# Optimization experiments

Measured on AMD Instinct MI355X. Metric: run time of the kernel, lower is better.

## Reference

```python
import jax, jax.numpy as jnp
import numpy as np

B, N, D, H, DM = 4, 1024, 1024, 16, 4096
DH = D // H
SCALE = DH ** -0.5
EPS = 1e-5


def layer_norm(x, g, b):
    mu = jnp.mean(x, axis=-1, keepdims=True)
    var = jnp.mean((x - mu) ** 2, axis=-1, keepdims=True)
    return (x - mu) * jax.lax.rsqrt(var + EPS) * g + b


def mha(q_in, k_in, v_in, Wq, bq, Wk, bk, Wv, bv, Wp, bp):
    # weights stored (in, out); torch Linear equivalent y = x @ W + b
    q = (q_in @ Wq + bq).reshape(B, -1, H, DH).transpose(0, 2, 1, 3)  # (B,H,Nq,DH)
    k = (k_in @ Wk + bk).reshape(B, -1, H, DH).transpose(0, 2, 1, 3)
    v = (v_in @ Wv + bv).reshape(B, -1, H, DH).transpose(0, 2, 1, 3)
    attn = jax.nn.softmax(jnp.einsum('bhqd,bhkd->bhqk', q, k) * SCALE, axis=-1)
    x = jnp.einsum('bhqk,bhkd->bhqd', attn, v).transpose(0, 2, 1, 3).reshape(B, -1, D)
    return x @ Wp + bp


def setup_inputs() -> dict:
    key = jax.random.key(0)
    ks = jax.random.split(key, 32)
    s = 0.02
    inp = {
        'tokens_enc': jax.random.normal(ks[0], (B, N, D), jnp.float32),
        'tokens_dec': jax.random.normal(ks[1], (B, N, D), jnp.float32),
        'PE_enc': jax.random.normal(ks[2], (B, N, D), jnp.float32),
        'PE_dec': jax.random.normal(ks[3], (B, N, D), jnp.float32),
    }
    names = ['sa_Wq', 'sa_Wk', 'sa_Wv', 'sa_Wp', 'ca_Wq', 'ca_Wk', 'ca_Wv', 'ca_Wp']
    for i, n in enumerate(names):
        inp[n] = jax.random.normal(ks[4 + i], (D, D), jnp.float32) * s
        inp[n.replace('W', 'b')] = jnp.zeros((D,), jnp.float32)
    inp['mlp_W1'] = jax.random.normal(ks[12], (D, DM), jnp.float32) * s
    inp['mlp_b1'] = jnp.zeros((DM,), jnp.float32)
    inp['mlp_W2'] = jax.random.normal(ks[13], (DM, D), jnp.float32) * s
    inp['mlp_b2'] = jnp.zeros((D,), jnp.float32)
    for i in (1, 2, 3):
        inp[f'ln{i}_g'] = jnp.ones((D,), jnp.float32)
        inp[f'ln{i}_b'] = jnp.zeros((D,), jnp.float32)
    return inp


def reference(tokens_enc, tokens_dec, PE_enc, PE_dec,
              sa_Wq, sa_bq, sa_Wk, sa_bk, sa_Wv, sa_bv, sa_Wp, sa_bp,
              ca_Wq, ca_bq, ca_Wk, ca_bk, ca_Wv, ca_bv, ca_Wp, ca_bp,
              mlp_W1, mlp_b1, mlp_W2, mlp_b2,
              ln1_g, ln1_b, ln2_g, ln2_b, ln3_g, ln3_b):
    # SA (pre-norm): q=k=ln(x)+PE_dec, v=ln(x)
    x2 = layer_norm(tokens_dec, ln1_g, ln1_b)
    qk = x2 + PE_dec
    tokens_dec = tokens_dec + mha(qk, qk, x2, sa_Wq, sa_bq, sa_Wk, sa_bk, sa_Wv, sa_bv, sa_Wp, sa_bp)
    # CA: q=ln(x)+PE_dec, k=enc+PE_enc, v=enc
    x2 = layer_norm(tokens_dec, ln2_g, ln2_b)
    tokens_dec = tokens_dec + mha(x2 + PE_dec, tokens_enc + PE_enc, tokens_enc,
                                  ca_Wq, ca_bq, ca_Wk, ca_bk, ca_Wv, ca_bv, ca_Wp, ca_bp)
    # FFD
    x2 = layer_norm(tokens_dec, ln3_g, ln3_b)
    h = jax.nn.gelu(x2 @ mlp_W1 + mlp_b1, approximate=False)
    return tokens_dec + (h @ mlp_W2 + mlp_b2)
```

## Files before the change

### kernel.cpp

```cpp
#include <hip/hip_runtime.h>
#include <hip/hip_bf16.h>
#include <math.h>

#define B_ 4
#define N_ 1024
#define D_ 1024
#define H_ 16
#define DH_ 64
#define DM_ 4096
#define NT_ (B_*N_)
#define EPS_ 1e-5f
#define SCALE_ 0.125f
#define CEXP_ 0.1803368801111244f

typedef unsigned short u16;
typedef short s16x8 __attribute__((ext_vector_type(8)));
typedef __bf16 y16x8 __attribute__((ext_vector_type(8)));
typedef float f32x4 __attribute__((ext_vector_type(4)));
typedef float f32x16 __attribute__((ext_vector_type(16)));

#define ZERO16 (f32x16){0.f,0.f,0.f,0.f,0.f,0.f,0.f,0.f,0.f,0.f,0.f,0.f,0.f,0.f,0.f,0.f}

__device__ __forceinline__ u16 f2bs(float f) {
  unsigned int u = __builtin_bit_cast(unsigned int, f);
  u += 0x7fffu + ((u >> 16) & 1u);
  return (u16)(u >> 16);
}

static __device__ __forceinline__ f32x4 MFMA(y16x8 a, y16x8 b, f32x4 c) {
  return __builtin_amdgcn_mfma_f32_16x16x32_bf16(a, b, c, 0, 0, 0);
}
static __device__ __forceinline__ f32x16 MFMA32(y16x8 a, y16x8 b, f32x16 c) {
  return __builtin_amdgcn_mfma_f32_32x32x16_bf16(a, b, c, 0, 0, 0);
}

static __device__ __forceinline__ unsigned cvtpk(float a, float b) {
  unsigned r;
  asm("v_cvt_pk_bf16_f32 %0, %1, %2" : "=v"(r) : "v"(a), "v"(b));
  return r;
}

static __device__ __forceinline__ void async16(void* lds, const void* g) {
  __builtin_amdgcn_global_load_lds(
      (const __attribute__((address_space(1))) unsigned int*)g,
      (__attribute__((address_space(3))) unsigned int*)lds, 16, 0, 0);
}

__global__ __launch_bounds__(256) void k_wtrans8(
    const float* __restrict__ s0, const float* __restrict__ s1,
    const float* __restrict__ s2, const float* __restrict__ s3,
    const float* __restrict__ s4, const float* __restrict__ s5,
    const float* __restrict__ s6, const float* __restrict__ s7,
    u16* __restrict__ dst) {
  const float* W = blockIdx.z == 0 ? s0 : blockIdx.z == 1 ? s1 : blockIdx.z == 2 ? s2
                 : blockIdx.z == 3 ? s3 : blockIdx.z == 4 ? s4 : blockIdx.z == 5 ? s5
                 : blockIdx.z == 6 ? s6 : s7;
  u16* Wt = dst + (size_t)blockIdx.z * D_ * D_;
  __shared__ u16 tile[32][33];
  int n0 = blockIdx.x * 32, k0 = blockIdx.y * 32;
  int tx = threadIdx.x & 31, ty = threadIdx.x >> 5;
#pragma unroll
  for (int i = 0; i < 4; ++i) {
    int k = k0 + ty + i * 8;
    tile[ty + i * 8][tx] = f2bs(W[(size_t)k * D_ + n0 + tx]);
  }
  __syncthreads();
#pragma unroll
  for (int i = 0; i < 4; ++i) {
    int n = n0 + ty + i * 8;
    Wt[(size_t)n * D_ + k0 + tx] = tile[tx][ty + i * 8];
  }
}

__global__ __launch_bounds__(256) void k_wtrans(const float* __restrict__ W,
                                                u16* __restrict__ Wt,
                                                int K, int Ncols) {
  __shared__ u16 tile[32][33];
  int n0 = blockIdx.x * 32, k0 = blockIdx.y * 32;
  int tx = threadIdx.x & 31, ty = threadIdx.x >> 5;
#pragma unroll
  for (int i = 0; i < 4; ++i) {
    int k = k0 + ty + i * 8;
    tile[ty + i * 8][tx] = f2bs(W[(size_t)k * Ncols + n0 + tx]);
  }
  __syncthreads();
#pragma unroll
  for (int i = 0; i < 4; ++i) {
    int n = n0 + ty + i * 8;
    Wt[(size_t)n * K + k0 + tx] = tile[tx][ty + i * 8];
  }
}

__global__ __launch_bounds__(256) void k_encprep(const float* __restrict__ enc,
                                                 const float* __restrict__ pe,
                                                 u16* __restrict__ encpe,
                                                 u16* __restrict__ encv) {
  int i = blockIdx.x * 256 + threadIdx.x;
  float4 e = ((const float4*)enc)[i];
  float4 p = ((const float4*)pe)[i];
  union { u16 u[4]; uint2 v; } a, b;
  a.u[0] = f2bs(e.x + p.x); a.u[1] = f2bs(e.y + p.y);
  a.u[2] = f2bs(e.z + p.z); a.u[3] = f2bs(e.w + p.w);
  b.u[0] = f2bs(e.x); b.u[1] = f2bs(e.y); b.u[2] = f2bs(e.z); b.u[3] = f2bs(e.w);
  ((uint2*)encpe)[i] = a.v;
  ((uint2*)encv)[i] = b.v;
}

__global__ __launch_bounds__(256) void k_ln(const float* __restrict__ x,
                                            const float* __restrict__ g,
                                            const float* __restrict__ bta,
                                            const float* __restrict__ pe,
                                            u16* __restrict__ x2o,
                                            u16* __restrict__ qko) {
  int row = blockIdx.x;
  int t = threadIdx.x;
  float4 v = ((const float4*)(x + (size_t)row * D_))[t];
  float s = v.x + v.y + v.z + v.w;
#pragma unroll
  for (int o = 1; o < 64; o <<= 1) s += __shfl_xor(s, o, 64);
  __shared__ float red[8];
  if ((t & 63) == 0) red[t >> 6] = s;
  __syncthreads();
  float mean = (red[0] + red[1] + red[2] + red[3]) * (1.0f / D_);
  float dx = v.x - mean, dy = v.y - mean, dz = v.z - mean, dw = v.w - mean;
  float s2 = dx * dx + dy * dy + dz * dz + dw * dw;
#pragma unroll
  for (int o = 1; o < 64; o <<= 1) s2 += __shfl_xor(s2, o, 64);
  if ((t & 63) == 0) red[4 + (t >> 6)] = s2;
  __syncthreads();
  float var = (red[4] + red[5] + red[6] + red[7]) * (1.0f / D_);
  float rstd = rsqrtf(var + EPS_);
  float4 gv = ((const float4*)g)[t];
  float4 bv = ((const float4*)bta)[t];
  float y0 = dx * rstd * gv.x + bv.x;
  float y1 = dy * rstd * gv.y + bv.y;
  float y2 = dz * rstd * gv.z + bv.z;
  float y3 = dw * rstd * gv.w + bv.w;
  union { u16 u[4]; uint2 v2; } o1;
  o1.u[0] = f2bs(y0); o1.u[1] = f2bs(y1); o1.u[2] = f2bs(y2); o1.u[3] = f2bs(y3);
  ((uint2*)(x2o + (size_t)row * D_))[t] = o1.v2;
  if (pe) {
    float4 pv = ((const float4*)(pe + (size_t)row * D_))[t];
    union { u16 u[4]; uint2 v2; } o2;
    o2.u[0] = f2bs(y0 + pv.x); o2.u[1] = f2bs(y1 + pv.y);
    o2.u[2] = f2bs(y2 + pv.z); o2.u[3] = f2bs(y3 + pv.w);
    ((uint2*)(qko + (size_t)row * D_))[t] = o2.v2;
  }
}

template <int EPI, int BM>
__global__ __launch_bounds__(512) void k_gemm(const u16* __restrict__ A,
                                              const u16* __restrict__ Bt,
                                              const float* __restrict__ bias,
                                              const float* __restrict__ res,
                                              float* __restrict__ outf,
                                              u16* __restrict__ outb,
                                              int M, int Nn, int K, int ldo) {
  constexpr int BN = 128, BK = 64;
  constexpr int FM = BM / 32;
  __shared__ __align__(128) char smem[2][(BM + BN) * BK * 2];
  const int t = threadIdx.x;
  const int wave = t >> 6, lane = t & 63, lg = lane >> 4, lc = lane & 15;
  const int nwg = gridDim.x * gridDim.y;
  const int bid = blockIdx.y * gridDim.x + blockIdx.x;
  const int lb = (bid & 7) * (nwg >> 3) + (bid >> 3);
  const int bx = lb % gridDim.x, by = lb / gridDim.x;
  const int m0 = by * BM, n0 = bx * BN;
  const int wm = (wave >> 2) * (BM / 2), wn = (wave & 3) * 32;
  f32x4 acc[FM][2];
#pragma unroll
  for (int i = 0; i < FM; ++i)
#pragma unroll
    for (int j = 0; j < 2; ++j) acc[i][j] = (f32x4){0.f, 0.f, 0.f, 0.f};
  const char* Ag = (const char*)(A + (size_t)m0 * K);
  const char* Bg = (const char*)(Bt + (size_t)n0 * K);
  const int sr = t >> 3, sp = t & 7;

  auto stage = [&](int bufi, int kt) {
    char* sA = smem[bufi];
    char* sB = smem[bufi] + BM * BK * 2;
#pragma unroll
    for (int rr = 0; rr < BM / 64; ++rr) {
      int row = rr * 64 + sr;
      int c = sp ^ (row & 7);
      async16(sA + (size_t)row * 128 + sp * 16,
              Ag + ((size_t)row * K + kt + c * 8) * 2);
    }
#pragma unroll
    for (int rr = 0; rr < 2; ++rr) {
      int row = rr * 64 + sr;
      int c = sp ^ (row & 7);
      async16(sB + (size_t)row * 128 + sp * 16,
              Bg + ((size_t)row * K + kt + c * 8) * 2);
    }
  };
  auto compute = [&](int bufi) {
    const char* sA = smem[bufi];
    const char* sB = smem[bufi] + BM * BK * 2;
#pragma unroll
    for (int ks = 0; ks < 2; ++ks) {
      y16x8 af[FM], bfr[2];
#pragma unroll
      for (int fm = 0; fm < FM; ++fm) {
        int R = wm + fm * 16 + lc;
        int pc = (ks * 4 + lg) ^ (R & 7);
        af[fm] = *(const y16x8*)(sA + (size_t)R * 128 + pc * 16);
      }
#pragma unroll
      for (int fn = 0; fn < 2; ++fn) {
        int R = wn + fn * 16 + lc;
        int pc = (ks * 4 + lg) ^ (R & 7);
        bfr[fn] = *(const y16x8*)(sB + (size_t)R * 128 + pc * 16);
      }
#pragma unroll
      for (int fm = 0; fm < FM; ++fm)
#pragma unroll
        for (int fn = 0; fn < 2; ++fn)
          acc[fm][fn] = MFMA(af[fm], bfr[fn], acc[fm][fn]);
    }
  };

  stage(0, 0);
  __syncthreads();
  int cur = 0;
  for (int kt = BK; kt < K; kt += BK) {
    stage(cur ^ 1, kt);
    compute(cur);
    __syncthreads();
    cur ^= 1;
  }
  compute(cur);

#pragma unroll
  for (int fm = 0; fm < FM; ++fm)
#pragma unroll
    for (int fn = 0; fn < 2; ++fn)
#pragma unroll
      for (int j = 0; j < 4; ++j) {
        int row = m0 + wm + fm * 16 + lg * 4 + j;
        int col = n0 + wn + fn * 16 + lc;
        float vv = acc[fm][fn][j] + bias[col];
        size_t idx = (size_t)row * ldo + col;
        if constexpr (EPI == 0) {
          outb[idx] = f2bs(vv);
        } else if constexpr (EPI == 1) {
          outf[idx] = vv + res[idx];
        } else {
          float gx = 0.5f * vv * (1.0f + erff(vv * 0.70710678118f));
          outb[idx] = f2bs(gx);
        }
      }
}

__global__ __launch_bounds__(512) void k_gemmG(
    const u16* __restrict__ A0, const u16* __restrict__ A1,
    const u16* __restrict__ A2, const u16* __restrict__ A3,
    const u16* __restrict__ A4, const u16* __restrict__ W0,
    const u16* __restrict__ W1, const u16* __restrict__ W2,
    const u16* __restrict__ W3, const u16* __restrict__ W4,
    const float* __restrict__ b0, const float* __restrict__ b1,
    const float* __restrict__ b2, const float* __restrict__ b3,
    const float* __restrict__ b4, u16* __restrict__ qk1,
    u16* __restrict__ vt1, u16* __restrict__ qk2, u16* __restrict__ vt2) {
  constexpr int BM = 128, BN = 128, BK = 64, K = D_;
  __shared__ __align__(128) char smem[2][(BM + BN) * BK * 2];
  const int z = blockIdx.z;
  const u16* A = z == 0 ? A0 : z == 1 ? A1 : z == 2 ? A2 : z == 3 ? A3 : A4;
  const u16* Bt = z == 0 ? W0 : z == 1 ? W1 : z == 2 ? W2 : z == 3 ? W3 : W4;
  const float* bias = z == 0 ? b0 : z == 1 ? b1 : z == 2 ? b2 : z == 3 ? b3 : b4;
  const int t = threadIdx.x;
  const int wave = t >> 6, lane = t & 63, lg = lane >> 4, lc = lane & 15;
  const int nwg = gridDim.x * gridDim.y;
  const int bid = blockIdx.y * gridDim.x + blockIdx.x;
  const int lb = (bid & 7) * (nwg >> 3) + (bid >> 3);
  const int bx = lb % gridDim.x, by = lb / gridDim.x;
  const int m0 = by * BM, n0 = bx * BN;
  const int wm = (wave >> 2) * 64, wn = (wave & 3) * 32;
  f32x4 acc[4][2];
#pragma unroll
  for (int i = 0; i < 4; ++i)
#pragma unroll
    for (int j = 0; j < 2; ++j) acc[i][j] = (f32x4){0.f, 0.f, 0.f, 0.f};
  const char* Ag = (const char*)(A + (size_t)m0 * K);
  const char* Bg = (const char*)(Bt + (size_t)n0 * K);
  const int sr = t >> 3, sp = t & 7;

  auto stage = [&](int bufi, int kt) {
    char* sA = smem[bufi];
    char* sB = smem[bufi] + BM * BK * 2;
#pragma unroll
    for (int rr = 0; rr < 2; ++rr) {
      int row = rr * 64 + sr;
      int c = sp ^ (row & 7);
      async16(sA + (size_t)row * 128 + sp * 16,
              Ag + ((size_t)row * K + kt + c * 8) * 2);
      async16(sB + (size_t)row * 128 + sp * 16,
              Bg + ((size_t)row * K + kt + c * 8) * 2);
    }
  };
  auto compute = [&](int bufi) {
    const char* sA = smem[bufi];
    const char* sB = smem[bufi] + BM * BK * 2;
#pragma unroll
    for (int ks = 0; ks < 2; ++ks) {
      y16x8 af[4], bfr[2];
#pragma unroll
      for (int fm = 0; fm < 4; ++fm) {
        int R = wm + fm * 16 + lc;
        int pc = (ks * 4 + lg) ^ (R & 7);
        af[fm] = *(const y16x8*)(sA + (size_t)R * 128 + pc * 16);
      }
#pragma unroll
      for (int fn = 0; fn < 2; ++fn) {
        int R = wn + fn * 16 + lc;
        int pc = (ks * 4 + lg) ^ (R & 7);
        bfr[fn] = *(const y16x8*)(sB + (size_t)R * 128 + pc * 16);
      }
#pragma unroll
      for (int fm = 0; fm < 4; ++fm)
#pragma unroll
        for (int fn = 0; fn < 2; ++fn)
          acc[fm][fn] = MFMA(af[fm], bfr[fn], acc[fm][fn]);
    }
  };

  stage(0, 0);
  __syncthreads();
  int cur = 0;
  for (int kt = BK; kt < K; kt += BK) {
    stage(cur ^ 1, kt);
    compute(cur);
    __syncthreads();
    cur ^= 1;
  }
  compute(cur);

  const bool isV = (z == 2) || (z == 4);
  if (!isV) {
    u16* outqk = (z == 3) ? qk2 : qk1;
    const int coff = (z == 1 || z == 3) ? D_ : 0;
#pragma unroll
    for (int fm = 0; fm < 4; ++fm)
#pragma unroll
      for (int fn = 0; fn < 2; ++fn)
#pragma unroll
        for (int j = 0; j < 4; ++j) {
          int row = m0 + wm + fm * 16 + lg * 4 + j;
          int col = n0 + wn + fn * 16 + lc;
          outqk[(size_t)row * (2 * D_) + coff + col] =
              f2bs(acc[fm][fn][j] + bias[col]);
        }
  } else {
    u16* outvt = (z == 2) ? vt1 : vt2;
#pragma unroll
    for (int fm = 0; fm < 4; ++fm)
#pragma unroll
      for (int fn = 0; fn < 2; ++fn) {
        int row0 = m0 + wm + fm * 16 + lg * 4;
        int col = n0 + wn + fn * 16 + lc;
        int bb = row0 >> 10, nn = row0 & (N_ - 1);
        int h = col >> 6, dh = col & 63;
        float bcol = bias[col];
        union { u16 u[4]; uint2 v; } pk;
#pragma unroll
        for (int j = 0; j < 4; ++j) pk.u[j] = f2bs(acc[fm][fn][j] + bcol);
        *(uint2*)&outvt[(((size_t)bb * H_ + h) * DH_ + dh) * N_ + nn] = pk.v;
      }
  }
}

__global__ __launch_bounds__(256) void k_attn(const u16* __restrict__ q, int qs,
                                              const u16* __restrict__ k, int ks2,
                                              const u16* __restrict__ vt,
                                              u16* __restrict__ out) {
  __shared__ __align__(16) u16 Kl[64][64];
  __shared__ __align__(16) u16 Vl[64][64];
  __shared__ __align__(16) u16 Ol[4][32][72];
  const int lb = blockIdx.x;
  const int bh = (lb & 7) | ((lb >> 6) << 3);
  const int qb = (lb >> 3) & 7;
  const int b = bh >> 4, h = bh & 15;
  const int t = threadIdx.x, wave = t >> 6, lane = t & 63;
  const int ql = lane & 31, hi = lane >> 5;
  const int q0 = qb * 128 + wave * 32;
  const u16* qp = q + ((size_t)b * N_ + q0) * qs + h * DH_;
  const u16* kp = k + (size_t)b * N_ * ks2 + h * DH_;
  const u16* vp = vt + ((size_t)bh * DH_) * N_;

  y16x8 aq[4];
#pragma unroll
  for (int s = 0; s < 4; ++s)
    aq[s] = *(const y16x8*)(qp + (size_t)ql * qs + s * 16 + hi * 8);

  f32x16 o0 = ZERO16, o1 = ZERO16;
  float m_r = -1e30f, l_r = 0.f;

  for (int kt = 0; kt < N_; kt += 64) {
    __syncthreads();
#pragma unroll
    for (int rr = 0; rr < 2; ++rr) {
      int id = rr * 256 + t;
      int row = id >> 3, c = id & 7;
      int pc2 = c ^ (row & 7);
      *(s16x8*)&Kl[row][pc2 * 8] =
          *(const s16x8*)(kp + (size_t)(kt + row) * ks2 + c * 8);
      *(s16x8*)&Vl[row][pc2 * 8] =
          *(const s16x8*)(vp + (size_t)row * N_ + kt + c * 8);
    }
    __syncthreads();

    f32x16 st0 = ZERO16, st1 = ZERO16;
#pragma unroll
    for (int s = 0; s < 4; ++s) {
      int pc0 = ((s * 2 + hi) ^ (ql & 7)) * 8;
      y16x8 ak0 = *(const y16x8*)&Kl[ql][pc0];
      y16x8 ak1 = *(const y16x8*)&Kl[32 + ql][pc0];
      st0 = MFMA32(ak0, aq[s], st0);
      st1 = MFMA32(ak1, aq[s], st1);
    }

    float mx = st0[0];
#pragma unroll
    for (int r = 1; r < 16; ++r) mx = fmaxf(mx, st0[r]);
#pragma unroll
    for (int r = 0; r < 16; ++r) mx = fmaxf(mx, st1[r]);
    mx = fmaxf(mx, __shfl_xor(mx, 32, 64));
    float mn = fmaxf(m_r, mx);
    float corr = exp2f((m_r - mn) * CEXP_);
    float ps = 0.f;
#pragma unroll
    for (int r = 0; r < 16; ++r) {
      float e = exp2f((st0[r] - mn) * CEXP_); st0[r] = e; ps += e;
    }
#pragma unroll
    for (int r = 0; r < 16; ++r) {
      float e = exp2f((st1[r] - mn) * CEXP_); st1[r] = e; ps += e;
    }
    ps += __shfl_xor(ps, 32, 64);
    l_r = l_r * corr + ps;
    m_r = mn;
    o0 = o0 * corr;
    o1 = o1 * corr;

#pragma unroll
    for (int ks = 0; ks < 4; ++ks) {
      unsigned A0, A1, B0, B1;
      if (ks < 2) {
        const int il = ks * 8;
        A0 = cvtpk(st0[il + 0], st0[il + 1]);
        A1 = cvtpk(st0[il + 2], st0[il + 3]);
        B0 = cvtpk(st0[il + 4], st0[il + 5]);
        B1 = cvtpk(st0[il + 6], st0[il + 7]);
      } else {
        const int il = (ks - 2) * 8;
        A0 = cvtpk(st1[il + 0], st1[il + 1]);
        A1 = cvtpk(st1[il + 2], st1[il + 3]);
        B0 = cvtpk(st1[il + 4], st1[il + 5]);
        B1 = cvtpk(st1[il + 6], st1[il + 7]);
      }
      asm("v_permlane32_swap_b32 %0, %1" : "+v"(A0), "+v"(B0));
      asm("v_permlane32_swap_b32 %0, %1" : "+v"(A1), "+v"(B1));
      union { unsigned w[4]; y16x8 v; } fr;
      fr.w[0] = A0; fr.w[1] = A1; fr.w[2] = B0; fr.w[3] = B1;
      int pc = ((ks * 2 + hi) ^ (ql & 7)) * 8;
      y16x8 bv0 = *(const y16x8*)&Vl[ql][pc];
      y16x8 bv1 = *(const y16x8*)&Vl[32 + ql][pc];
      o0 = MFMA32(bv0, fr.v, o0);
      o1 = MFMA32(bv1, fr.v, o1);
    }
  }

  float rl = 1.f / l_r;
#pragma unroll
  for (int rq = 0; rq < 4; ++rq)
#pragma unroll
    for (int e = 0; e < 4; e += 2) {
      *(unsigned*)&Ol[wave][ql][8 * rq + 4 * hi + e] =
          cvtpk(o0[rq * 4 + e] * rl, o0[rq * 4 + e + 1] * rl);
      *(unsigned*)&Ol[wave][ql][32 + 8 * rq + 4 * hi + e] =
          cvtpk(o1[rq * 4 + e] * rl, o1[rq * 4 + e + 1] * rl);
    }
#pragma unroll
  for (int pp = 0; pp < 4; ++pp) {
    int row = pp * 8 + (lane >> 3);
    s16x8 vv = *(const s16x8*)&Ol[wave][row][(lane & 7) * 8];
    *(s16x8*)(out + ((size_t)b * N_ + q0 + row) * D_ + h * DH_ + (lane & 7) * 8) = vv;
  }
}

extern "C" void kernel_launch(void* const* d_in, const int* in_sizes, int n_in,
                              void* d_out, int out_size, void* d_ws, size_t ws_size,
                              hipStream_t stream) {
  const float* tokens_enc = (const float*)d_in[0];
  const float* tokens_dec = (const float*)d_in[1];
  const float* PE_enc = (const float*)d_in[2];
  const float* PE_dec = (const float*)d_in[3];
  const float* sa_Wq = (const float*)d_in[4];  const float* sa_bq = (const float*)d_in[5];
  const float* sa_Wk = (const float*)d_in[6];  const float* sa_bk = (const float*)d_in[7];
  const float* sa_Wv = (const float*)d_in[8];  const float* sa_bv = (const float*)d_in[9];
  const float* sa_Wp = (const float*)d_in[10]; const float* sa_bp = (const float*)d_in[11];
  const float* ca_Wq = (const float*)d_in[12]; const float* ca_bq = (const float*)d_in[13];
  const float* ca_Wk = (const float*)d_in[14]; const float* ca_bk = (const float*)d_in[15];
  const float* ca_Wv = (const float*)d_in[16]; const float* ca_bv = (const float*)d_in[17];
  const float* ca_Wp = (const float*)d_in[18]; const float* ca_bp = (const float*)d_in[19];
  const float* mlp_W1 = (const float*)d_in[20]; const float* mlp_b1 = (const float*)d_in[21];
  const float* mlp_W2 = (const float*)d_in[22]; const float* mlp_b2 = (const float*)d_in[23];
  const float* ln1_g = (const float*)d_in[24]; const float* ln1_b = (const float*)d_in[25];
  const float* ln2_g = (const float*)d_in[26]; const float* ln2_b = (const float*)d_in[27];
  const float* ln3_g = (const float*)d_in[28]; const float* ln3_b = (const float*)d_in[29];

  char* wsp = (char*)d_ws;
  size_t off = 0;
  auto alloc = [&](size_t bytes) -> char* {
    char* p = wsp + off;
    off += (bytes + 255) & ~(size_t)255;
    return p;
  };
  u16* w8   = (u16*)alloc((size_t)8 * D_ * D_ * 2);
  u16* w1T  = (u16*)alloc((size_t)DM_ * D_ * 2);
  u16* w2T  = (u16*)alloc((size_t)D_ * DM_ * 2);
  u16* encpe = (u16*)alloc((size_t)NT_ * D_ * 2);
  u16* encv  = (u16*)alloc((size_t)NT_ * D_ * 2);
  u16* x2b = (u16*)alloc((size_t)NT_ * D_ * 2);
  u16* qkb = (u16*)alloc((size_t)NT_ * D_ * 2);
  u16* qkm = (u16*)alloc((size_t)NT_ * 2 * D_ * 2);
  u16* qkm2 = (u16*)alloc((size_t)NT_ * 2 * D_ * 2);
  u16* vtb = (u16*)alloc((size_t)NT_ * D_ * 2);
  u16* vtb2 = (u16*)alloc((size_t)NT_ * D_ * 2);
  u16* attb = (u16*)alloc((size_t)NT_ * D_ * 2);
  float* dec1 = (float*)alloc((size_t)NT_ * D_ * 4);
  float* dec2 = (float*)alloc((size_t)NT_ * D_ * 4);
  u16* hb = (u16*)alloc((size_t)NT_ * DM_ * 2);

  const size_t DD = (size_t)D_ * D_;
  u16* wqT  = w8;
  u16* wkT  = w8 + 1 * DD;
  u16* wvT  = w8 + 2 * DD;
  u16* wpT  = w8 + 3 * DD;
  u16* cwqT = w8 + 4 * DD;
  u16* cwkT = w8 + 5 * DD;
  u16* cwvT = w8 + 6 * DD;
  u16* cwpT = w8 + 7 * DD;

  k_wtrans8<<<dim3(32, 32, 8), 256, 0, stream>>>(sa_Wq, sa_Wk, sa_Wv, sa_Wp,
                                                 ca_Wq, ca_Wk, ca_Wv, ca_Wp, w8);
  k_wtrans<<<dim3(128, 32), 256, 0, stream>>>(mlp_W1, w1T, D_, DM_);
  k_wtrans<<<dim3(32, 128), 256, 0, stream>>>(mlp_W2, w2T, DM_, D_);
  k_encprep<<<dim3(NT_ * D_ / 1024), 256, 0, stream>>>(tokens_enc, PE_enc, encpe, encv);

  k_ln<<<dim3(NT_), 256, 0, stream>>>(tokens_dec, ln1_g, ln1_b, PE_dec, x2b, qkb);
  k_gemmG<<<dim3(8, 32, 5), 512, 0, stream>>>(
      qkb, qkb, x2b, encpe, encv, wqT, wkT, wvT, cwkT, cwvT,
      sa_bq, sa_bk, sa_bv, ca_bk, ca_bv, qkm, vtb, qkm2, vtb2);
  k_attn<<<dim3(512), 256, 0, stream>>>(qkm, 2 * D_, qkm + D_, 2 * D_, vtb, attb);
  k_gemm<1, 64><<<dim3(8, 64), 512, 0, stream>>>(attb, wpT, sa_bp, tokens_dec,
                                                 dec1, nullptr, NT_, D_, D_, D_);

  k_ln<<<dim3(NT_), 256, 0, stream>>>(dec1, ln2_g, ln2_b, PE_dec, x2b, qkb);
  k_gemm<0, 64><<<dim3(8, 64), 512, 0, stream>>>(qkb, cwqT, ca_bq, nullptr,
                                                 nullptr, qkm2, NT_, D_, D_, 2 * D_);
  k_attn<<<dim3(512), 256, 0, stream>>>(qkm2, 2 * D_, qkm2 + D_, 2 * D_, vtb2, attb);
  k_gemm<1, 64><<<dim3(8, 64), 512, 0, stream>>>(attb, cwpT, ca_bp, dec1,
                                                 dec2, nullptr, NT_, D_, D_, D_);

  k_ln<<<dim3(NT_), 256, 0, stream>>>(dec2, ln3_g, ln3_b, nullptr, x2b, nullptr);
  k_gemm<2, 128><<<dim3(32, 32), 512, 0, stream>>>(x2b, w1T, mlp_b1, nullptr,
                                                   nullptr, hb, NT_, DM_, D_, DM_);
  k_gemm<1, 64><<<dim3(8, 64), 512, 0, stream>>>(hb, w2T, mlp_b2, dec2,
                                                 (float*)d_out, nullptr, NT_, D_, DM_, D_);
}
```

Baseline: 350.4 us.

## Prefetch next K/V tile into registers and lazily rescale softmax in attention

```diff
diff --git a/kernel.cpp b/kernel.cpp
--- a/kernel.cpp
+++ b/kernel.cpp
@@ -395,21 +395,36 @@
   f32x16 o0 = ZERO16, o1 = ZERO16;
   float m_r = -1e30f, l_r = 0.f;
 
+  const int srow0 = t >> 3, sc = t & 7;
+  s16x8 kreg[2], vreg[2];
+#pragma unroll
+  for (int rr = 0; rr < 2; ++rr) {
+    int row = rr * 32 + srow0;
+    kreg[rr] = *(const s16x8*)(kp + (size_t)row * ks2 + sc * 8);
+    vreg[rr] = *(const s16x8*)(vp + (size_t)row * N_ + sc * 8);
+  }
+
   for (int kt = 0; kt < N_; kt += 64) {
     __syncthreads();
 #pragma unroll
     for (int rr = 0; rr < 2; ++rr) {
-      int id = rr * 256 + t;
-      int row = id >> 3, c = id & 7;
-      int pc2 = c ^ (row & 7);
-      *(s16x8*)&Kl[row][pc2 * 8] =
-          *(const s16x8*)(kp + (size_t)(kt + row) * ks2 + c * 8);
-      *(s16x8*)&Vl[row][pc2 * 8] =
-          *(const s16x8*)(vp + (size_t)row * N_ + kt + c * 8);
+      int row = rr * 32 + srow0;
+      int pc2 = sc ^ (row & 7);
+      *(s16x8*)&Kl[row][pc2 * 8] = kreg[rr];
+      *(s16x8*)&Vl[row][pc2 * 8] = vreg[rr];
     }
     __syncthreads();
+    if (kt + 64 < N_) {
+#pragma unroll
+      for (int rr = 0; rr < 2; ++rr) {
+        int row = rr * 32 + srow0;
+        kreg[rr] = *(const s16x8*)(kp + (size_t)(kt + 64 + row) * ks2 + sc * 8);
+        vreg[rr] = *(const s16x8*)(vp + (size_t)row * N_ + kt + 64 + sc * 8);
+      }
+    }
 
     f32x16 st0 = ZERO16, st1 = ZERO16;
+    __builtin_amdgcn_s_setprio(1);
 #pragma unroll
     for (int s = 0; s < 4; ++s) {
       int pc0 = ((s * 2 + hi) ^ (ql & 7)) * 8;
@@ -418,6 +433,7 @@
       st0 = MFMA32(ak0, aq[s], st0);
       st1 = MFMA32(ak1, aq[s], st1);
     }
+    __builtin_amdgcn_s_setprio(0);
 
     float mx = st0[0];
 #pragma unroll
@@ -425,23 +441,27 @@
 #pragma unroll
     for (int r = 0; r < 16; ++r) mx = fmaxf(mx, st1[r]);
     mx = fmaxf(mx, __shfl_xor(mx, 32, 64));
-    float mn = fmaxf(m_r, mx);
-    float corr = exp2f((m_r - mn) * CEXP_);
+    if (!__all(mx - m_r <= 32.f)) {
+      float mn = fmaxf(m_r, mx);
+      float corr = exp2f((m_r - mn) * CEXP_);
+      l_r *= corr;
+      o0 = o0 * corr;
+      o1 = o1 * corr;
+      m_r = mn;
+    }
     float ps = 0.f;
 #pragma unroll
     for (int r = 0; r < 16; ++r) {
-      float e = exp2f((st0[r] - mn) * CEXP_); st0[r] = e; ps += e;
+      float e = exp2f((st0[r] - m_r) * CEXP_); st0[r] = e; ps += e;
     }
 #pragma unroll
     for (int r = 0; r < 16; ++r) {
-      float e = exp2f((st1[r] - mn) * CEXP_); st1[r] = e; ps += e;
+      float e = exp2f((st1[r] - m_r) * CEXP_); st1[r] = e; ps += e;
     }
     ps += __shfl_xor(ps, 32, 64);
-    l_r = l_r * corr + ps;
-    m_r = mn;
-    o0 = o0 * corr;
-    o1 = o1 * corr;
-
+    l_r += ps;
+
+    __builtin_amdgcn_s_setprio(1);
 #pragma unroll
     for (int ks = 0; ks < 4; ++ks) {
       unsigned A0, A1, B0, B1;
@@ -468,6 +488,7 @@
       o0 = MFMA32(bv0, fr.v, o0);
       o1 = MFMA32(bv1, fr.v, o1);
     }
+    __builtin_amdgcn_s_setprio(0);
   }
 
   float rl = 1.f / l_r;
```

New measurement: 336.7 us. -3.9%, faster.
